# Performance work log

Measured on AMD Instinct MI355X. Metric: run time of the kernel, lower is better.

Reference implementation:

```python
import jax, jax.numpy as jnp
import numpy as np

N, C, T, V = 64, 64, 256, 25
REL, OUT = 8, 64
ALPHA = 1.0


def setup_inputs() -> dict:
    key = jax.random.key(0)
    ks = jax.random.split(key, 10)
    s = lambda k, shape: jax.random.normal(k, shape, dtype=jnp.float32) * 0.05
    return {
        "x": jax.random.normal(ks[0], (N, C, T, V), dtype=jnp.float32),
        "A": jax.random.normal(ks[1], (V, V), dtype=jnp.float32),
        "w1": s(ks[2], (REL, C)), "b1": s(ks[3], (REL,)),
        "w2": s(ks[4], (REL, C)), "b2": s(ks[5], (REL,)),
        "w3": s(ks[6], (OUT, C)), "b3": s(ks[7], (OUT,)),
        "w4": s(ks[8], (OUT, REL)), "b4": s(ks[9], (OUT,)),
    }


def reference(x, A, w1, b1, w2, b2, w3, b3, w4, b4):
    # 1x1 conv commutes with the temporal mean, so reduce T first (same math).
    xm = jnp.mean(x, axis=2)                                   # [N, C, V]
    x1 = jnp.einsum('ncv,rc->nrv', xm, w1) + b1[:, None]        # [N, R, V]
    x2 = jnp.einsum('ncv,rc->nrv', xm, w2) + b2[:, None]        # [N, R, V]
    x3 = jnp.einsum('nctv,oc->notv', x, w3) + b3[:, None, None] # [N, O, T, V]
    # dynamic topology: tanh of broadcast difference -> [N, R, V, V]
    adj = jnp.tanh(x1[:, :, :, None] - x2[:, :, None, :])
    # conv4 (1x1 over VxV) then scale + static adjacency
    d = jnp.einsum('nruv,or->nouv', adj, w4) + b4[:, None, None]
    d = d * ALPHA + A[None, None]                               # [N, O, V, V]
    # graph aggregation: out[n,o,t,v] = sum_u d[n,o,u,v] * x3[n,o,t,u]
    return jnp.einsum('nouv,notu->notv', d, x3)
```

## Files before the change

kernel.cpp:

```cpp
#include <hip/hip_runtime.h>

#define N_ 64
#define C_ 64
#define T_ 256
#define V_ 25
#define R_ 8
#define O_ 64
constexpr int TV = T_ * V_;
constexpr float INV_T = 1.0f / (float)T_;
constexpr int TC = 16;
constexpr int UP = 40;
constexpr int DP = 32;

typedef __attribute__((ext_vector_type(8))) short s8v;
typedef __attribute__((ext_vector_type(4))) float f4v;

__device__ __forceinline__ unsigned short f2bf(float f) {
    union { float f; unsigned u; } v; v.f = f;
    unsigned r = v.u + 0x7FFFu + ((v.u >> 16) & 1u);
    return (unsigned short)(r >> 16);
}

__global__ __launch_bounds__(256) void k_mean(const float* __restrict__ x,
                                              float* __restrict__ xm) {
    __shared__ float part[8 * V_];
    const int bid = blockIdx.x;
    const int tid = threadIdx.x;
    const float* xp = x + (size_t)bid * TV;
    if (tid < 200) {
        const int vid = tid % V_;
        const int seg = tid / V_;
        float s = 0.f;
        const float* p = xp + seg * 32 * V_ + vid;
        #pragma unroll
        for (int j = 0; j < 32; ++j) s += p[j * V_];
        part[tid] = s;
    }
    __syncthreads();
    if (tid < V_) {
        float s = 0.f;
        #pragma unroll
        for (int k = 0; k < 8; ++k) s += part[k * V_ + tid];
        xm[(size_t)bid * V_ + tid] = s * INV_T;
    }
}

__global__ __launch_bounds__(256) void k_dmat(const float* __restrict__ xm,
                                              const float* __restrict__ A,
                                              const float* __restrict__ w1,
                                              const float* __restrict__ b1,
                                              const float* __restrict__ w2,
                                              const float* __restrict__ b2,
                                              const float* __restrict__ w4,
                                              const float* __restrict__ b4,
                                              unsigned short* __restrict__ dT) {
    __shared__ float xms[C_][V_];
    __shared__ float x1s[R_][V_];
    __shared__ float x2s[R_][V_];
    const int n  = blockIdx.x;
    const int og = blockIdx.y * 16;
    const int tid = threadIdx.x;

    for (int i = tid; i < C_ * V_; i += 256)
        xms[i / V_][i % V_] = xm[(size_t)n * C_ * V_ + i];
    __syncthreads();

    for (int i = tid; i < 2 * R_ * V_; i += 256) {
        const int j = i % (R_ * V_);
        const int r = j / V_, v = j % V_;
        const bool first = (i < R_ * V_);
        const float* w = first ? w1 : w2;
        float acc = first ? b1[r] : b2[r];
        #pragma unroll
        for (int c = 0; c < C_; ++c) acc += w[r * C_ + c] * xms[c][v];
        if (first) x1s[r][v] = acc;
        else       x2s[r][v] = acc;
    }
    __syncthreads();

    unsigned short* dn = dT + (size_t)n * O_ * DP * DP;
    for (int p = tid; p < DP * DP; p += 256) {
        const int v = p >> 5, u = p & 31;
        if (u < V_ && v < V_) {
            float adjr[R_];
            #pragma unroll
            for (int r = 0; r < R_; ++r) adjr[r] = tanhf(x1s[r][u] - x2s[r][v]);
            const float a = A[u * V_ + v];
            #pragma unroll
            for (int oo = 0; oo < 16; ++oo) {
                const int o = og + oo;
                float acc = b4[o];
                #pragma unroll
                for (int r = 0; r < R_; ++r) acc = fmaf(w4[o * R_ + r], adjr[r], acc);
                dn[(size_t)o * DP * DP + p] = f2bf(acc + a);
            }
        } else {
            #pragma unroll
            for (int oo = 0; oo < 16; ++oo)
                dn[(size_t)(og + oo) * DP * DP + p] = 0;
        }
    }
}

__global__ __launch_bounds__(512, 4) void k_F(const float* __restrict__ x,
                                              const float* __restrict__ w3,
                                              const float* __restrict__ b3,
                                              const unsigned short* __restrict__ dT,
                                              float* __restrict__ out) {
    __shared__ __align__(16) unsigned short x3b[O_][TC][UP];

    const int n    = blockIdx.y;
    const int tc   = blockIdx.x;
    const int tid  = threadIdx.x;
    const int lane = tid & 63;
    const int wave = tid >> 6;
    const int l16  = lane & 15;
    const int lg   = lane >> 4;

    #pragma unroll
    for (int p = 0; p < 2; ++p) {
        const int pair = tid + 512 * p;
        const int o = pair >> 4, t = pair & 15;
        #pragma unroll
        for (int u = 25; u < 32; ++u) x3b[o][t][u] = 0;
    }

    s8v afr[4][2];
    #pragma unroll
    for (int m = 0; m < 4; ++m) {
        #pragma unroll
        for (int kh = 0; kh < 2; ++kh) {
            const float* wp = w3 + (m * 16 + l16) * C_ + kh * 32 + lg * 8;
            s8v f;
            #pragma unroll
            for (int j = 0; j < 8; ++j) f[j] = (short)f2bf(wp[j]);
            afr[m][kh] = f;
        }
    }
    f4v b3r[4];
    #pragma unroll
    for (int m = 0; m < 4; ++m)
        b3r[m] = *(const f4v*)(b3 + m * 16 + lg * 4);

    const float* xbase = x + (size_t)n * C_ * TV + tc * (TC * V_);
    #pragma unroll 1
    for (int i = 0; i < 4; ++i) {
        const int nt = wave + 8 * i;
        if (nt < 25) {
            const int pos = nt * 16 + l16;
            const int t = pos / 25, u = pos - 25 * t;
            s8v bfr[2];
            #pragma unroll
            for (int kh = 0; kh < 2; ++kh) {
                s8v f;
                #pragma unroll
                for (int j = 0; j < 8; ++j)
                    f[j] = (short)f2bf(xbase[(size_t)(kh * 32 + lg * 8 + j) * TV + pos]);
                bfr[kh] = f;
            }
            #pragma unroll
            for (int m = 0; m < 4; ++m) {
                f4v acc = (f4v)0.f;
                acc = __builtin_amdgcn_mfma_f32_16x16x32_bf16(afr[m][0], bfr[0], acc, 0, 0, 0);
                acc = __builtin_amdgcn_mfma_f32_16x16x32_bf16(afr[m][1], bfr[1], acc, 0, 0, 0);
                #pragma unroll
                for (int r = 0; r < 4; ++r)
                    x3b[m * 16 + lg * 4 + r][t][u] = f2bf(acc[r] + b3r[m][r]);
            }
        }
    }
    __syncthreads();

    const unsigned short* dn = dT + (size_t)n * O_ * DP * DP;
    float* on = out + (size_t)n * O_ * TV + tc * (TC * V_);
    #pragma unroll
    for (int oo = 0; oo < 8; ++oo) {
        const int o = wave * 8 + oo;
        const unsigned short* dp = dn + (size_t)o * DP * DP;
        const s8v bv0 = *(const s8v*)(dp + l16 * DP + lg * 8);
        const s8v bv1 = *(const s8v*)(dp + (16 + l16) * DP + lg * 8);
        const s8v av  = *(const s8v*)&x3b[o][l16][lg * 8];
        f4v c0 = (f4v)0.f, c1 = (f4v)0.f;
        c0 = __builtin_amdgcn_mfma_f32_16x16x32_bf16(av, bv0, c0, 0, 0, 0);
        c1 = __builtin_amdgcn_mfma_f32_16x16x32_bf16(av, bv1, c1, 0, 0, 0);
        float* ob = on + (size_t)o * TV;
        #pragma unroll
        for (int r = 0; r < 4; ++r) {
            const int t = lg * 4 + r;
            ob[t * 25 + l16] = c0[r];
            if (l16 < 9) ob[t * 25 + 16 + l16] = c1[r];
        }
    }
}

extern "C" void kernel_launch(void* const* d_in, const int* in_sizes, int n_in,
                              void* d_out, int out_size, void* d_ws, size_t ws_size,
                              hipStream_t stream) {
    const float* x  = (const float*)d_in[0];
    const float* A  = (const float*)d_in[1];
    const float* w1 = (const float*)d_in[2];
    const float* b1 = (const float*)d_in[3];
    const float* w2 = (const float*)d_in[4];
    const float* b2 = (const float*)d_in[5];
    const float* w3 = (const float*)d_in[6];
    const float* b3 = (const float*)d_in[7];
    const float* w4 = (const float*)d_in[8];
    const float* b4 = (const float*)d_in[9];

    float* out = (float*)d_out;
    float* xm  = (float*)d_ws;
    unsigned short* dTm = (unsigned short*)(xm + (size_t)N_ * C_ * V_);

    k_mean<<<N_ * C_, 256, 0, stream>>>(x, xm);
    k_dmat<<<dim3(N_, 4), 256, 0, stream>>>(xm, A, w1, b1, w2, b2, w4, b4, dTm);
    k_F<<<dim3(T_ / TC, N_), 512, 0, stream>>>(x, w3, b3, dTm, out);
}
```

Baseline: 84.65 us.

## Stage x tile in LDS with coalesced float4 loads and process outputs in chunks

```diff
diff --git a/kernel.cpp b/kernel.cpp
--- a/kernel.cpp
+++ b/kernel.cpp
@@ -9,10 +9,14 @@
 constexpr int TV = T_ * V_;
 constexpr float INV_T = 1.0f / (float)T_;
 constexpr int TC = 16;
-constexpr int UP = 40;
+constexpr int NPOS = TC * V_;
+constexpr int NT = NPOS / 16;
 constexpr int DP = 32;
+constexpr int UPAD = 40;
+constexpr int X3S = 16 * UPAD + 8;
 
 typedef __attribute__((ext_vector_type(8))) short s8v;
+typedef __attribute__((ext_vector_type(4))) short s4v;
 typedef __attribute__((ext_vector_type(4))) float f4v;
 
 __device__ __forceinline__ unsigned short f2bf(float f) {
@@ -58,7 +62,7 @@
     __shared__ float x1s[R_][V_];
     __shared__ float x2s[R_][V_];
     const int n  = blockIdx.x;
-    const int og = blockIdx.y * 16;
+    const int og = blockIdx.y * 8;
     const int tid = threadIdx.x;
 
     for (int i = tid; i < C_ * V_; i += 256)
@@ -87,7 +91,7 @@
             for (int r = 0; r < R_; ++r) adjr[r] = tanhf(x1s[r][u] - x2s[r][v]);
             const float a = A[u * V_ + v];
             #pragma unroll
-            for (int oo = 0; oo < 16; ++oo) {
+            for (int oo = 0; oo < 8; ++oo) {
                 const int o = og + oo;
                 float acc = b4[o];
                 #pragma unroll
@@ -96,7 +100,7 @@
             }
         } else {
             #pragma unroll
-            for (int oo = 0; oo < 16; ++oo)
+            for (int oo = 0; oo < 8; ++oo)
                 dn[(size_t)(og + oo) * DP * DP + p] = 0;
         }
     }
@@ -107,7 +111,8 @@
                                               const float* __restrict__ b3,
                                               const unsigned short* __restrict__ dT,
                                               float* __restrict__ out) {
-    __shared__ __align__(16) unsigned short x3b[O_][TC][UP];
+    __shared__ __align__(16) unsigned short xs[NT * 1024];
+    __shared__ __align__(16) unsigned short x3b[16 * X3S];
 
     const int n    = blockIdx.y;
     const int tc   = blockIdx.x;
@@ -117,79 +122,103 @@
     const int l16  = lane & 15;
     const int lg   = lane >> 4;
 
+    if (tid < 256) {
+        const int o_l = tid >> 4, t = tid & 15;
+        *(s8v*)&x3b[o_l * X3S + t * UPAD + 24] = (s8v)0;
+    }
+
+    {
+        const float* xb = x + (size_t)n * C_ * TV + tc * NPOS;
+        #pragma unroll 1
+        for (int i = 0; i < 13; ++i) {
+            const int s = i * 512 + tid;
+            if (s < 6400) {
+                const int c = s / 100, p4 = s - c * 100;
+                const float4 v4 = *(const float4*)(xb + (size_t)c * TV + p4 * 4);
+                const int pos = p4 * 4;
+                const int pt = pos >> 4;
+                s4v pk;
+                pk[0] = (short)f2bf(v4.x); pk[1] = (short)f2bf(v4.y);
+                pk[2] = (short)f2bf(v4.z); pk[3] = (short)f2bf(v4.w);
+                *(s4v*)&xs[pt * 1024 + ((c ^ (pt & 7)) << 4) + (pos & 15)] = pk;
+            }
+        }
+    }
+    __syncthreads();
+
+    s8v bfr[4][2];
+    int ts[4], us[4];
     #pragma unroll
-    for (int p = 0; p < 2; ++p) {
-        const int pair = tid + 512 * p;
-        const int o = pair >> 4, t = pair & 15;
-        #pragma unroll
-        for (int u = 25; u < 32; ++u) x3b[o][t][u] = 0;
-    }
-
-    s8v afr[4][2];
-    #pragma unroll
-    for (int m = 0; m < 4; ++m) {
-        #pragma unroll
-        for (int kh = 0; kh < 2; ++kh) {
-            const float* wp = w3 + (m * 16 + l16) * C_ + kh * 32 + lg * 8;
-            s8v f;
-            #pragma unroll
-            for (int j = 0; j < 8; ++j) f[j] = (short)f2bf(wp[j]);
-            afr[m][kh] = f;
-        }
-    }
-    f4v b3r[4];
-    #pragma unroll
-    for (int m = 0; m < 4; ++m)
-        b3r[m] = *(const f4v*)(b3 + m * 16 + lg * 4);
-
-    const float* xbase = x + (size_t)n * C_ * TV + tc * (TC * V_);
-    #pragma unroll 1
     for (int i = 0; i < 4; ++i) {
         const int nt = wave + 8 * i;
-        if (nt < 25) {
+        if (nt < NT) {
             const int pos = nt * 16 + l16;
-            const int t = pos / 25, u = pos - 25 * t;
-            s8v bfr[2];
+            ts[i] = pos / 25; us[i] = pos - 25 * ts[i];
+            const unsigned short* base = &xs[nt * 1024];
+            const int sw = nt & 7;
             #pragma unroll
             for (int kh = 0; kh < 2; ++kh) {
                 s8v f;
                 #pragma unroll
-                for (int j = 0; j < 8; ++j)
-                    f[j] = (short)f2bf(xbase[(size_t)(kh * 32 + lg * 8 + j) * TV + pos]);
-                bfr[kh] = f;
-            }
-            #pragma unroll
-            for (int m = 0; m < 4; ++m) {
+                for (int j = 0; j < 8; ++j) {
+                    const int c = kh * 32 + lg * 8 + j;
+                    f[j] = (short)base[((c ^ sw) << 4) + l16];
+                }
+                bfr[i][kh] = f;
+            }
+        }
+    }
+
+    const unsigned short* dn = dT + (size_t)n * O_ * DP * DP;
+    float* on = out + (size_t)n * O_ * TV + tc * NPOS;
+
+    #pragma unroll 1
+    for (int h = 0; h < 4; ++h) {
+        s8v afr[2];
+        #pragma unroll
+        for (int kh = 0; kh < 2; ++kh) {
+            const float* wp = w3 + (h * 16 + l16) * C_ + kh * 32 + lg * 8;
+            s8v f;
+            #pragma unroll
+            for (int j = 0; j < 8; ++j) f[j] = (short)f2bf(wp[j]);
+            afr[kh] = f;
+        }
+        const f4v b3h = *(const f4v*)(b3 + h * 16 + lg * 4);
+
+        #pragma unroll
+        for (int i = 0; i < 4; ++i) {
+            const int nt = wave + 8 * i;
+            if (nt < NT) {
                 f4v acc = (f4v)0.f;
-                acc = __builtin_amdgcn_mfma_f32_16x16x32_bf16(afr[m][0], bfr[0], acc, 0, 0, 0);
-                acc = __builtin_amdgcn_mfma_f32_16x16x32_bf16(afr[m][1], bfr[1], acc, 0, 0, 0);
+                acc = __builtin_amdgcn_mfma_f32_16x16x32_bf16(afr[0], bfr[i][0], acc, 0, 0, 0);
+                acc = __builtin_amdgcn_mfma_f32_16x16x32_bf16(afr[1], bfr[i][1], acc, 0, 0, 0);
                 #pragma unroll
                 for (int r = 0; r < 4; ++r)
-                    x3b[m * 16 + lg * 4 + r][t][u] = f2bf(acc[r] + b3r[m][r]);
-            }
-        }
-    }
-    __syncthreads();
-
-    const unsigned short* dn = dT + (size_t)n * O_ * DP * DP;
-    float* on = out + (size_t)n * O_ * TV + tc * (TC * V_);
-    #pragma unroll
-    for (int oo = 0; oo < 8; ++oo) {
-        const int o = wave * 8 + oo;
-        const unsigned short* dp = dn + (size_t)o * DP * DP;
-        const s8v bv0 = *(const s8v*)(dp + l16 * DP + lg * 8);
-        const s8v bv1 = *(const s8v*)(dp + (16 + l16) * DP + lg * 8);
-        const s8v av  = *(const s8v*)&x3b[o][l16][lg * 8];
-        f4v c0 = (f4v)0.f, c1 = (f4v)0.f;
-        c0 = __builtin_amdgcn_mfma_f32_16x16x32_bf16(av, bv0, c0, 0, 0, 0);
-        c1 = __builtin_amdgcn_mfma_f32_16x16x32_bf16(av, bv1, c1, 0, 0, 0);
-        float* ob = on + (size_t)o * TV;
-        #pragma unroll
-        for (int r = 0; r < 4; ++r) {
-            const int t = lg * 4 + r;
-            ob[t * 25 + l16] = c0[r];
-            if (l16 < 9) ob[t * 25 + 16 + l16] = c1[r];
-        }
+                    x3b[(lg * 4 + r) * X3S + ts[i] * UPAD + us[i]] = f2bf(acc[r] + b3h[r]);
+            }
+        }
+        __syncthreads();
+
+        #pragma unroll
+        for (int oo = 0; oo < 2; ++oo) {
+            const int o_l = wave * 2 + oo;
+            const int o_g = h * 16 + o_l;
+            const s8v av  = *(const s8v*)&x3b[o_l * X3S + l16 * UPAD + lg * 8];
+            const unsigned short* dp = dn + (size_t)o_g * DP * DP;
+            const s8v bv0 = *(const s8v*)(dp + l16 * DP + lg * 8);
+            const s8v bv1 = *(const s8v*)(dp + (16 + l16) * DP + lg * 8);
+            f4v c0 = (f4v)0.f, c1 = (f4v)0.f;
+            c0 = __builtin_amdgcn_mfma_f32_16x16x32_bf16(av, bv0, c0, 0, 0, 0);
+            c1 = __builtin_amdgcn_mfma_f32_16x16x32_bf16(av, bv1, c1, 0, 0, 0);
+            float* ob = on + (size_t)o_g * TV;
+            #pragma unroll
+            for (int r = 0; r < 4; ++r) {
+                const int t = lg * 4 + r;
+                ob[t * 25 + l16] = c0[r];
+                if (l16 < 9) ob[t * 25 + 16 + l16] = c1[r];
+            }
+        }
+        __syncthreads();
     }
 }
 
@@ -212,6 +241,6 @@
     unsigned short* dTm = (unsigned short*)(xm + (size_t)N_ * C_ * V_);
 
     k_mean<<<N_ * C_, 256, 0, stream>>>(x, xm);
-    k_dmat<<<dim3(N_, 4), 256, 0, stream>>>(xm, A, w1, b1, w2, b2, w4, b4, dTm);
+    k_dmat<<<dim3(N_, 8), 256, 0, stream>>>(xm, A, w1, b1, w2, b2, w4, b4, dTm);
     k_F<<<dim3(T_ / TC, N_), 512, 0, stream>>>(x, w3, b3, dTm, out);
 }
```

Result: slower. 88.46 us (+4.5%).
